# Kernel tuning notes

Hardware: AMD Instinct MI355X
Metric: run time of the kernel (lower is better)

## Reference

```python
import jax, jax.numpy as jnp
import numpy as np

EPS = 1e-5

def _conv3x3(x, w):
    # x: [N,C,H,W], w: [O,I,3,3], stride 1, padding 1
    return jax.lax.conv_general_dilated(
        x, w, window_strides=(1, 1), padding=((1, 1), (1, 1)),
        dimension_numbers=('NCHW', 'OIHW', 'NCHW'))

def _bn(x, gamma, beta, rmean, rvar):
    # inference-mode BatchNorm2d over channel dim
    scale = gamma * jax.lax.rsqrt(rvar + EPS)
    return x * scale[None, :, None, None] + (beta - rmean * scale)[None, :, None, None]

def setup_inputs() -> dict:
    key = jax.random.key(0)
    ks = jax.random.split(key, 8)
    N, C, H, W = 32, 256, 56, 56
    x = jax.random.normal(ks[0], (N, C, H, W), dtype=jnp.float32)
    w1 = jax.random.normal(ks[1], (C, C, 3, 3), dtype=jnp.float32) * 0.05
    w2 = jax.random.normal(ks[2], (C, C, 3, 3), dtype=jnp.float32) * 0.05
    g1 = jax.random.normal(ks[3], (C,), dtype=jnp.float32) * 0.1 + 1.0
    b1 = jax.random.normal(ks[4], (C,), dtype=jnp.float32) * 0.1
    g2 = jax.random.normal(ks[5], (C,), dtype=jnp.float32) * 0.1 + 1.0
    b2 = jax.random.normal(ks[6], (C,), dtype=jnp.float32) * 0.1
    rm1 = jax.random.normal(jax.random.fold_in(key, 10), (C,), dtype=jnp.float32) * 0.1
    rv1 = jax.random.uniform(jax.random.fold_in(key, 11), (C,), dtype=jnp.float32) + 0.5
    rm2 = jax.random.normal(jax.random.fold_in(key, 12), (C,), dtype=jnp.float32) * 0.1
    rv2 = jax.random.uniform(jax.random.fold_in(key, 13), (C,), dtype=jnp.float32) + 0.5
    return {'x': x, 'w1': w1, 'g1': g1, 'b1': b1, 'rm1': rm1, 'rv1': rv1,
            'w2': w2, 'g2': g2, 'b2': b2, 'rm2': rm2, 'rv2': rv2}

def reference(x, w1, g1, b1, rm1, rv1, w2, g2, b2, rm2, rv2):
    identity = x
    out = jax.nn.relu(_bn(_conv3x3(x, w1), g1, b1, rm1, rv1))
    out = _bn(_conv3x3(out, w2), g2, b2, rm2, rv2)
    return jax.nn.relu(out + identity)
```

## Files before the change

### kernel.cpp

```cpp
#include <hip/hip_runtime.h>
#include <hip/hip_bf16.h>

#define NN 32
#define CC 256
#define HH 56
#define WW 56
#define HP 58
#define PIX (HH * WW)
#define MTOT (NN * PIX)
#define BN_EPS 1e-5f

using f32x4  = __attribute__((ext_vector_type(4))) float;
using short8 = __attribute__((ext_vector_type(8))) short;

__device__ __forceinline__ void gload16(const void* g, void* l) {
    __builtin_amdgcn_global_load_lds(
        (const __attribute__((address_space(1))) void*)g,
        (__attribute__((address_space(3))) void*)l, 16, 0, 0);
}


__global__ __launch_bounds__(256) void transform_x(const float* __restrict__ x,
                                                   __hip_bfloat16* __restrict__ xt) {
    __shared__ float t[64][65];
    const int tx = threadIdx.x & 63, ty = threadIdx.x >> 6;
    const int c0 = blockIdx.x * 64, h = blockIdx.y, n = blockIdx.z;
    #pragma unroll
    for (int i = 0; i < 16; ++i) {
        const int c = ty + i * 4;
        float v = 0.f;
        if (tx < WW) v = x[(((size_t)n * CC + c0 + c) * HH + h) * WW + tx];
        t[c][tx] = v;
    }
    __syncthreads();
    #pragma unroll
    for (int i = 0; i < 16; ++i) {
        const int w = ty + i * 4;
        if (w < WW)
            xt[((n * HP + h + 1) * HP + (w + 1)) * CC + c0 + tx] = __float2bfloat16(t[tx][w]);
    }
}

__global__ void transform_w(const float* __restrict__ w, __hip_bfloat16* __restrict__ wt) {
    const int co = blockIdx.x, tap = blockIdx.y, ci = threadIdx.x;
    wt[(tap * CC + co) * CC + ci] = __float2bfloat16(w[(co * CC + ci) * 9 + tap]);
}

__global__ void zero_borders(__hip_bfloat16* __restrict__ buf) {
    const int i = blockIdx.x, n = blockIdx.y;
    int h, w;
    if (i < 58)       { h = 0;              w = i; }
    else if (i < 116) { h = 57;             w = i - 58; }
    else if (i < 172) { h = 1 + (i - 116);  w = 0; }
    else              { h = 1 + (i - 172);  w = 57; }
    buf[((n * HP + h) * HP + w) * CC + threadIdx.x] = __float2bfloat16(0.f);
}

template<bool SECOND>
__global__ __launch_bounds__(256, 4) void conv_mfma(
    const __hip_bfloat16* __restrict__ act,
    const __hip_bfloat16* __restrict__ wt,
    const float* __restrict__ g, const float* __restrict__ bb,
    const float* __restrict__ rm, const float* __restrict__ rv,
    const float* __restrict__ identity,
    void* __restrict__ out)
{
    __shared__ short As[128 * 64];
    __shared__ short Bs[128 * 64];

    const int tid  = threadIdx.x;
    const int lane = tid & 63;
    const int wid  = tid >> 6;
    const int wm = wid >> 1, wn = wid & 1;

    const int bid     = blockIdx.x;
    const int logical = (bid & 7) * 196 + (bid >> 3);
    const int nb = logical & 1;
    const int mb = logical >> 1;

    const int scol = (lane & 7) ^ (lane >> 3);

    int abase[4], bbase[4];
    #pragma unroll
    for (int j = 0; j < 4; ++j) {
        const int r = wid * 32 + j * 8 + (lane >> 3);
        const int p = mb * 128 + r;
        const int n   = p / PIX;
        const int rem = p - n * PIX;
        const int h = rem / WW, w = rem - h * WW;
        abase[j] = (((n * HP + h) * HP + w) * CC + scol * 8) * 2;
        const int co = nb * 128 + r;
        bbase[j] = (co * CC + scol * 8) * 2;
    }

    f32x4 acc[4][4];
    #pragma unroll
    for (int i = 0; i < 4; ++i)
        #pragma unroll
        for (int j = 0; j < 4; ++j)
            acc[i][j] = (f32x4){0.f, 0.f, 0.f, 0.f};

    const char* actB = (const char*)act;
    const char* wtB  = (const char*)wt;
    char* AsL = (char*)As;
    char* BsL = (char*)Bs;

    const int rlane = lane & 15;
    const int xorb  = (rlane & 7) << 4;
    const int colb  = (lane >> 4) << 4;

    for (int cic = 0; cic < 4; ++cic) {
        #pragma unroll
        for (int tap = 0; tap < 9; ++tap) {
            const int dh = tap / 3, dw = tap - dh * 3;
            const int aoff = (dh * HP + dw) * (CC * 2) + cic * 128;
            const int boff = tap * (CC * CC * 2) + cic * 128;
            #pragma unroll
            for (int j = 0; j < 4; ++j) {
                gload16(actB + abase[j] + aoff, AsL + wid * 4096 + j * 1024);
                gload16(wtB  + bbase[j] + boff, BsL + wid * 4096 + j * 1024);
            }
            __syncthreads();
            __builtin_amdgcn_s_setprio(1);
            #pragma unroll
            for (int ks = 0; ks < 2; ++ks) {
                const int coladdr = (ks * 64 + colb) ^ xorb;
                short8 a[4], bq[4];
                #pragma unroll
                for (int mf = 0; mf < 4; ++mf)
                    a[mf] = *(const short8*)(AsL + (wm * 64 + mf * 16 + rlane) * 128 + coladdr);
                #pragma unroll
                for (int nf = 0; nf < 4; ++nf)
                    bq[nf] = *(const short8*)(BsL + (wn * 64 + nf * 16 + rlane) * 128 + coladdr);
                #pragma unroll
                for (int mf = 0; mf < 4; ++mf)
                    #pragma unroll
                    for (int nf = 0; nf < 4; ++nf)
                        acc[mf][nf] = __builtin_amdgcn_mfma_f32_16x16x32_bf16(
                            a[mf], bq[nf], acc[mf][nf], 0, 0, 0);
            }
            __builtin_amdgcn_s_setprio(0);
            __syncthreads();
        }
    }

    const int lm = lane >> 4, ln = lane & 15;
    #pragma unroll
    for (int nf = 0; nf < 4; ++nf) {
        const int co = nb * 128 + wn * 64 + nf * 16 + ln;
        const float scale = g[co] * rsqrtf(rv[co] + BN_EPS);
        const float bias  = bb[co] - rm[co] * scale;
        #pragma unroll
        for (int mf = 0; mf < 4; ++mf) {
            const int p0  = mb * 128 + wm * 64 + mf * 16 + lm * 4;
            const int n   = p0 / PIX;
            const int pr  = p0 - n * PIX;
            f32x4 v = acc[mf][nf];
            if (SECOND) {
                const size_t off = (size_t)(n * CC + co) * PIX + pr;
                const float4 id = *(const float4*)(identity + off);
                float4 o;
                o.x = fmaxf(fmaf(v[0], scale, bias) + id.x, 0.f);
                o.y = fmaxf(fmaf(v[1], scale, bias) + id.y, 0.f);
                o.z = fmaxf(fmaf(v[2], scale, bias) + id.z, 0.f);
                o.w = fmaxf(fmaf(v[3], scale, bias) + id.w, 0.f);
                *(float4*)((float*)out + off) = o;
            } else {
                const int h = pr / WW, w = pr - h * WW;
                __hip_bfloat16* yp = (__hip_bfloat16*)out
                    + ((n * HP + h + 1) * HP + (w + 1)) * CC + co;
                #pragma unroll
                for (int r = 0; r < 4; ++r)
                    yp[r * CC] = __float2bfloat16(fmaxf(fmaf(v[r], scale, bias), 0.f));
            }
        }
    }
}

__device__ __forceinline__ float rb_(float v) { return __bfloat162float(__float2bfloat16(v)); }

template<bool SECOND>
__global__ __launch_bounds__(256) void conv_bn_naive(
    const void* __restrict__ in_v, const float* __restrict__ wmat,
    const float* __restrict__ g, const float* __restrict__ b,
    const float* __restrict__ rm, const float* __restrict__ rv,
    const float* __restrict__ identity, void* __restrict__ out_v)
{
    constexpr int CI_CHUNK = 8;
    __shared__ float xs[CI_CHUNK][3][58];
    __shared__ float ws_s[4][CI_CHUNK][9];
    const int tid = threadIdx.x;
    const int co_l = tid >> 6;
    const int wl_raw = tid & 63;
    const int wl = wl_raw < (WW - 1) ? wl_raw : (WW - 1);
    const int co = blockIdx.x * 4 + co_l;
    const int h = blockIdx.y, n = blockIdx.z;
    const float* in_f = (const float*)in_v;
    const __hip_bfloat16* in_b = (const __hip_bfloat16*)in_v;
    float acc = 0.f;
    for (int ci0 = 0; ci0 < CC; ci0 += CI_CHUNK) {
        __syncthreads();
        for (int i = tid; i < CI_CHUNK * 3 * 58; i += 256) {
            int ci = i / 174, rem = i - ci * 174, r = rem / 58, col = rem - r * 58;
            int h_in = h + r - 1, x_col = col - 1;
            float v = 0.f;
            if ((unsigned)h_in < HH && (unsigned)x_col < WW) {
                int idx = ((n * CC + ci0 + ci) * HH + h_in) * WW + x_col;
                v = SECOND ? __bfloat162float(in_b[idx]) : rb_(in_f[idx]);
            }
            xs[ci][r][col] = v;
        }
        for (int i = tid; i < 4 * CI_CHUNK * 9; i += 256) {
            int c_l = i / (CI_CHUNK * 9), rem = i - c_l * (CI_CHUNK * 9);
            int ci = rem / 9, k = rem - ci * 9;
            ws_s[c_l][ci][k] = rb_(wmat[(blockIdx.x * 4 + c_l) * CC * 9 + (ci0 + ci) * 9 + k]);
        }
        __syncthreads();
        #pragma unroll
        for (int ci = 0; ci < CI_CHUNK; ++ci) {
            float wr[9];
            #pragma unroll
            for (int k = 0; k < 9; ++k) wr[k] = ws_s[co_l][ci][k];
            #pragma unroll
            for (int dh = 0; dh < 3; ++dh)
                #pragma unroll
                for (int dw = 0; dw < 3; ++dw)
                    acc += xs[ci][dh][wl + dw] * wr[dh * 3 + dw];
        }
    }
    if (wl_raw < WW) {
        float scale = g[co] * rsqrtf(rv[co] + BN_EPS);
        float bias = b[co] - rm[co] * scale;
        float v = acc * scale + bias;
        int oidx = ((n * CC + co) * HH + h) * WW + wl_raw;
        if (SECOND) {
            v += identity[oidx];
            ((float*)out_v)[oidx] = fmaxf(v, 0.f);
        } else {
            ((__hip_bfloat16*)out_v)[oidx] = __float2bfloat16(fmaxf(v, 0.f));
        }
    }
}

extern "C" void kernel_launch(void* const* d_in, const int* in_sizes, int n_in,
                              void* d_out, int out_size, void* d_ws, size_t ws_size,
                              hipStream_t stream) {
    const float* x   = (const float*)d_in[0];
    const float* w1  = (const float*)d_in[1];
    const float* g1  = (const float*)d_in[2];
    const float* b1  = (const float*)d_in[3];
    const float* rm1 = (const float*)d_in[4];
    const float* rv1 = (const float*)d_in[5];
    const float* w2  = (const float*)d_in[6];
    const float* g2  = (const float*)d_in[7];
    const float* b2  = (const float*)d_in[8];
    const float* rm2 = (const float*)d_in[9];
    const float* rv2 = (const float*)d_in[10];

    const size_t XT_B = (size_t)NN * HP * HP * CC * 2;
    const size_t WT_B = (size_t)9 * CC * CC * 2;
    const size_t NEED = 2 * XT_B + 2 * WT_B;

    if (ws_size < NEED) {
        __hip_bfloat16* tmp = (__hip_bfloat16*)d_ws;
        dim3 grid(CC / 4, HH, NN);
        conv_bn_naive<false><<<grid, 256, 0, stream>>>(x, w1, g1, b1, rm1, rv1, nullptr, tmp);
        conv_bn_naive<true ><<<grid, 256, 0, stream>>>(tmp, w2, g2, b2, rm2, rv2, x, d_out);
        return;
    }

    char* ws = (char*)d_ws;
    __hip_bfloat16* xt  = (__hip_bfloat16*)ws;
    __hip_bfloat16* y1  = (__hip_bfloat16*)(ws + XT_B);
    __hip_bfloat16* wt1 = (__hip_bfloat16*)(ws + 2 * XT_B);
    __hip_bfloat16* wt2 = (__hip_bfloat16*)(ws + 2 * XT_B + WT_B);

    zero_borders<<<dim3(228, NN), 256, 0, stream>>>(xt);
    zero_borders<<<dim3(228, NN), 256, 0, stream>>>(y1);
    transform_x <<<dim3(4, HH, NN), 256, 0, stream>>>(x, xt);
    transform_w <<<dim3(CC, 9), 256, 0, stream>>>(w1, wt1);
    transform_w <<<dim3(CC, 9), 256, 0, stream>>>(w2, wt2);

    conv_mfma<false><<<1568, 256, 0, stream>>>(xt, wt1, g1, b1, rm1, rv1, nullptr, y1);
    conv_mfma<true ><<<1568, 256, 0, stream>>>(y1, wt2, g2, b2, rm2, rv2, x, d_out);
}
```

Before: 314.5 us.

## Use 256x256 tiles with double-buffered LDS pipelining in conv MFMA kernel

The implicit-GEMM conv kernel now uses 512-thread blocks, each computing a 256-pixel by 256-channel tile, which doubles per-wave work and cuts the grid to 392 blocks. Shared memory is double-buffered (128 KB): loads for the next tap and channel chunk are issued in four phases that interleave with MFMA work, with explicit vmcnt waits and barriers replacing the two syncthreads per step. This aims to hide global-to-LDS latency and raise reuse of each loaded tile. The cost is heavy LDS use and larger accumulator register pressure, allowing only one block per CU, and 392 blocks may not fill all CUs evenly.

```diff
diff --git a/kernel.cpp b/kernel.cpp
--- a/kernel.cpp
+++ b/kernel.cpp
@@ -57,7 +57,7 @@
 }
 
 template<bool SECOND>
-__global__ __launch_bounds__(256, 4) void conv_mfma(
+__global__ __launch_bounds__(512, 2) void conv_mfma(
     const __hip_bfloat16* __restrict__ act,
     const __hip_bfloat16* __restrict__ wt,
     const float* __restrict__ g, const float* __restrict__ bb,
@@ -65,94 +65,128 @@
     const float* __restrict__ identity,
     void* __restrict__ out)
 {
-    __shared__ short As[128 * 64];
-    __shared__ short Bs[128 * 64];
+    __shared__ short S[2][2][256][64];
+    char* SB = (char*)S;
 
     const int tid  = threadIdx.x;
     const int lane = tid & 63;
     const int wid  = tid >> 6;
-    const int wm = wid >> 1, wn = wid & 1;
-
-    const int bid     = blockIdx.x;
-    const int logical = (bid & 7) * 196 + (bid >> 3);
-    const int nb = logical & 1;
-    const int mb = logical >> 1;
+    const int wm   = wid >> 2;
+    const int wn   = wid & 3;
+
+    const int bid = blockIdx.x;
+    const int mb  = (bid & 7) * 49 + (bid >> 3);
 
     const int scol = (lane & 7) ^ (lane >> 3);
 
-    int abase[4], bbase[4];
-    #pragma unroll
-    for (int j = 0; j < 4; ++j) {
-        const int r = wid * 32 + j * 8 + (lane >> 3);
-        const int p = mb * 128 + r;
-        const int n   = p / PIX;
-        const int rem = p - n * PIX;
-        const int h = rem / WW, w = rem - h * WW;
-        abase[j] = (((n * HP + h) * HP + w) * CC + scol * 8) * 2;
-        const int co = nb * 128 + r;
-        bbase[j] = (co * CC + scol * 8) * 2;
-    }
-
-    f32x4 acc[4][4];
-    #pragma unroll
-    for (int i = 0; i < 4; ++i)
+    int abase[2][2], bbase[2][2];
+    #pragma unroll
+    for (int h2 = 0; h2 < 2; ++h2)
+        #pragma unroll
+        for (int j = 0; j < 2; ++j) {
+            const int r = h2 * 128 + j * 64 + wid * 8 + (lane >> 3);
+            const int p = mb * 256 + r;
+            const int n   = p / PIX;
+            const int rem = p - n * PIX;
+            const int h = rem / WW, w = rem - h * WW;
+            abase[h2][j] = (((n * HP + h) * HP + w) * CC + scol * 8) * 2;
+            bbase[h2][j] = (r * CC + scol * 8) * 2;
+        }
+
+    f32x4 acc[8][4];
+    #pragma unroll
+    for (int i = 0; i < 8; ++i)
         #pragma unroll
         for (int j = 0; j < 4; ++j)
             acc[i][j] = (f32x4){0.f, 0.f, 0.f, 0.f};
 
     const char* actB = (const char*)act;
     const char* wtB  = (const char*)wt;
-    char* AsL = (char*)As;
-    char* BsL = (char*)Bs;
+
+    auto stageA = [&](int buf, int h2, int t) {
+        const int cic = t / 9, tap = t - cic * 9;
+        const int dh = tap / 3, dw = tap - dh * 3;
+        const int aoff = (dh * HP + dw) * (CC * 2) + cic * 128;
+        char* dst = SB + buf * 65536 + h2 * 16384 + wid * 1024;
+        gload16(actB + abase[h2][0] + aoff, dst);
+        gload16(actB + abase[h2][1] + aoff, dst + 8192);
+    };
+    auto stageB = [&](int buf, int h2, int t) {
+        const int cic = t / 9, tap = t - cic * 9;
+        const int boff = tap * (CC * CC * 2) + cic * 128;
+        char* dst = SB + buf * 65536 + 32768 + h2 * 16384 + wid * 1024;
+        gload16(wtB + bbase[h2][0] + boff, dst);
+        gload16(wtB + bbase[h2][1] + boff, dst + 8192);
+    };
 
     const int rlane = lane & 15;
     const int xorb  = (rlane & 7) << 4;
     const int colb  = (lane >> 4) << 4;
 
-    for (int cic = 0; cic < 4; ++cic) {
-        #pragma unroll
-        for (int tap = 0; tap < 9; ++tap) {
-            const int dh = tap / 3, dw = tap - dh * 3;
-            const int aoff = (dh * HP + dw) * (CC * 2) + cic * 128;
-            const int boff = tap * (CC * CC * 2) + cic * 128;
+    stageA(0, 0, 0); stageA(0, 1, 0); stageB(0, 0, 0); stageB(0, 1, 0);
+
+    short8 bfr[2][4];
+
+    #pragma unroll 1
+    for (int t = 0; t < 36; ++t) {
+        const int cur = t & 1;
+        const bool last = (t == 35);
+        const char* Ab = SB + cur * 65536;
+        const char* Bb = SB + cur * 65536 + 32768;
+        #pragma unroll
+        for (int p = 0; p < 4; ++p) {
+            if (!last) {
+                if      (p == 0) stageA(cur ^ 1, 0, t + 1);
+                else if (p == 1) stageA(cur ^ 1, 1, t + 1);
+                else if (p == 2) stageB(cur ^ 1, 0, t + 1);
+                else             stageB(cur ^ 1, 1, t + 1);
+            }
+            if (p == 0) {
+                if (!last) asm volatile("s_waitcnt vmcnt(2)" ::: "memory");
+                else       asm volatile("s_waitcnt vmcnt(0)" ::: "memory");
+                __builtin_amdgcn_s_barrier();
+                __builtin_amdgcn_sched_barrier(0);
+            }
+            const int coladdr = ((p & 1) * 64 + colb) ^ xorb;
+            short8 afr[4];
             #pragma unroll
-            for (int j = 0; j < 4; ++j) {
-                gload16(actB + abase[j] + aoff, AsL + wid * 4096 + j * 1024);
-                gload16(wtB  + bbase[j] + boff, BsL + wid * 4096 + j * 1024);
-            }
-            __syncthreads();
+            for (int mi = 0; mi < 4; ++mi)
+                afr[mi] = *(const short8*)(Ab
+                    + (wm * 128 + ((p >> 1) * 4 + mi) * 16 + rlane) * 128 + coladdr);
+            if (p < 2) {
+                #pragma unroll
+                for (int nf = 0; nf < 4; ++nf)
+                    bfr[p][nf] = *(const short8*)(Bb
+                        + (wn * 64 + nf * 16 + rlane) * 128 + coladdr);
+            }
+            if (p != 0) {
+                __builtin_amdgcn_sched_barrier(0);
+                __builtin_amdgcn_s_barrier();
+                __builtin_amdgcn_sched_barrier(0);
+            }
             __builtin_amdgcn_s_setprio(1);
             #pragma unroll
-            for (int ks = 0; ks < 2; ++ks) {
-                const int coladdr = (ks * 64 + colb) ^ xorb;
-                short8 a[4], bq[4];
-                #pragma unroll
-                for (int mf = 0; mf < 4; ++mf)
-                    a[mf] = *(const short8*)(AsL + (wm * 64 + mf * 16 + rlane) * 128 + coladdr);
+            for (int mi = 0; mi < 4; ++mi)
                 #pragma unroll
                 for (int nf = 0; nf < 4; ++nf)
-                    bq[nf] = *(const short8*)(BsL + (wn * 64 + nf * 16 + rlane) * 128 + coladdr);
-                #pragma unroll
-                for (int mf = 0; mf < 4; ++mf)
-                    #pragma unroll
-                    for (int nf = 0; nf < 4; ++nf)
-                        acc[mf][nf] = __builtin_amdgcn_mfma_f32_16x16x32_bf16(
-                            a[mf], bq[nf], acc[mf][nf], 0, 0, 0);
-            }
+                    acc[(p >> 1) * 4 + mi][nf] = __builtin_amdgcn_mfma_f32_16x16x32_bf16(
+                        afr[mi], bfr[p & 1][nf], acc[(p >> 1) * 4 + mi][nf], 0, 0, 0);
             __builtin_amdgcn_s_setprio(0);
-            __syncthreads();
+            __builtin_amdgcn_sched_barrier(0);
+            __builtin_amdgcn_s_barrier();
+            __builtin_amdgcn_sched_barrier(0);
         }
     }
 
     const int lm = lane >> 4, ln = lane & 15;
     #pragma unroll
     for (int nf = 0; nf < 4; ++nf) {
-        const int co = nb * 128 + wn * 64 + nf * 16 + ln;
+        const int co = wn * 64 + nf * 16 + ln;
         const float scale = g[co] * rsqrtf(rv[co] + BN_EPS);
         const float bias  = bb[co] - rm[co] * scale;
         #pragma unroll
-        for (int mf = 0; mf < 4; ++mf) {
-            const int p0  = mb * 128 + wm * 64 + mf * 16 + lm * 4;
+        for (int mf = 0; mf < 8; ++mf) {
+            const int p0  = mb * 256 + wm * 128 + mf * 16 + lm * 4;
             const int n   = p0 / PIX;
             const int pr  = p0 - n * PIX;
             f32x4 v = acc[mf][nf];
@@ -281,6 +315,6 @@
     transform_w <<<dim3(CC, 9), 256, 0, stream>>>(w1, wt1);
     transform_w <<<dim3(CC, 9), 256, 0, stream>>>(w2, wt2);
 
-    conv_mfma<false><<<1568, 256, 0, stream>>>(xt, wt1, g1, b1, rm1, rv1, nullptr, y1);
-    conv_mfma<true ><<<1568, 256, 0, stream>>>(y1, wt2, g2, b2, rm2, rv2, x, d_out);
-}
+    conv_mfma<false><<<392, 512, 0, stream>>>(xt, wt1, g1, b1, rm1, rv1, nullptr, y1);
+    conv_mfma<true ><<<392, 512, 0, stream>>>(y1, wt2, g2, b2, rm2, rv2, x, d_out);
+}
```

Result: slower. 353.1 us (+12.3%).

## Double-buffer LDS tiles with half-depth K chunks to overlap loads and MFMA

Applied to the files above, without the earlier changes.

Splits each K step from 64 to 32 input channels and uses two LDS buffers of the same total size, so the global-to-LDS load for the next (channel chunk, tap) step is issued before computing on the current buffer. This drops one barrier per step and hides global load latency behind MFMA work, with a new swizzled LDS layout to match. In exchange it doubles the number of iterations, and with them the barrier count and loop overhead, and each step has less compute to cover the load.

```diff
diff --git a/kernel.cpp b/kernel.cpp
--- a/kernel.cpp
+++ b/kernel.cpp
@@ -65,8 +65,7 @@
     const float* __restrict__ identity,
     void* __restrict__ out)
 {
-    __shared__ short As[128 * 64];
-    __shared__ short Bs[128 * 64];
+    __shared__ char LDSm[32768];
 
     const int tid  = threadIdx.x;
     const int lane = tid & 63;
@@ -78,19 +77,20 @@
     const int nb = logical & 1;
     const int mb = logical >> 1;
 
-    const int scol = (lane & 7) ^ (lane >> 3);
-
-    int abase[4], bbase[4];
-    #pragma unroll
-    for (int j = 0; j < 4; ++j) {
-        const int r = wid * 32 + j * 8 + (lane >> 3);
-        const int p = mb * 128 + r;
+    const int u_s = (lane & 7) ^ (lane >> 3);
+    const int q_s = u_s & 3;
+
+    int abase[2], bbase[2];
+    #pragma unroll
+    for (int j = 0; j < 2; ++j) {
+        const int prow = wid * 32 + j * 16 + 2 * (lane >> 3) + (u_s >> 2);
+        const int p = mb * 128 + prow;
         const int n   = p / PIX;
         const int rem = p - n * PIX;
         const int h = rem / WW, w = rem - h * WW;
-        abase[j] = (((n * HP + h) * HP + w) * CC + scol * 8) * 2;
-        const int co = nb * 128 + r;
-        bbase[j] = (co * CC + scol * 8) * 2;
+        abase[j] = (((n * HP + h) * HP + w) * CC) * 2 + q_s * 16;
+        const int co = nb * 128 + prow;
+        bbase[j] = co * (CC * 2) + q_s * 16;
     }
 
     f32x4 acc[4][4];
@@ -102,44 +102,55 @@
 
     const char* actB = (const char*)act;
     const char* wtB  = (const char*)wt;
-    char* AsL = (char*)As;
-    char* BsL = (char*)Bs;
-
-    const int rlane = lane & 15;
-    const int xorb  = (rlane & 7) << 4;
-    const int colb  = (lane >> 4) << 4;
-
-    for (int cic = 0; cic < 4; ++cic) {
-        #pragma unroll
-        for (int tap = 0; tap < 9; ++tap) {
-            const int dh = tap / 3, dw = tap - dh * 3;
-            const int aoff = (dh * HP + dw) * (CC * 2) + cic * 128;
-            const int boff = tap * (CC * CC * 2) + cic * 128;
+
+    auto stage = [&](int bufSel, int cic, int tap) {
+        const int dh = tap / 3, dw = tap - dh * 3;
+        const int aoff = (dh * HP + dw) * (CC * 2) + cic * 64;
+        const int boff = tap * (CC * CC * 2) + cic * 64;
+        char* da = LDSm + bufSel * 8192 + wid * 2048;
+        char* db = LDSm + 16384 + bufSel * 8192 + wid * 2048;
+        #pragma unroll
+        for (int j = 0; j < 2; ++j) {
+            gload16(actB + abase[j] + aoff, da + j * 1024);
+            gload16(wtB  + bbase[j] + boff, db + j * 1024);
+        }
+    };
+
+    const int qr = lane >> 4, rr = lane & 15;
+    const int rb_l = ((rr >> 1) << 7) + (((((rr & 1) << 2) + qr) ^ (rr >> 1)) << 4);
+
+    auto compute = [&](int bufSel) {
+        const char* Ab = LDSm + bufSel * 8192;
+        const char* Bb = LDSm + 16384 + bufSel * 8192;
+        short8 a[4], bq[4];
+        #pragma unroll
+        for (int mf = 0; mf < 4; ++mf)
+            a[mf] = *(const short8*)(Ab + wm * 4096 + mf * 1024 + rb_l);
+        #pragma unroll
+        for (int nf = 0; nf < 4; ++nf)
+            bq[nf] = *(const short8*)(Bb + wn * 4096 + nf * 1024 + rb_l);
+        __builtin_amdgcn_s_setprio(1);
+        #pragma unroll
+        for (int mf = 0; mf < 4; ++mf)
             #pragma unroll
-            for (int j = 0; j < 4; ++j) {
-                gload16(actB + abase[j] + aoff, AsL + wid * 4096 + j * 1024);
-                gload16(wtB  + bbase[j] + boff, BsL + wid * 4096 + j * 1024);
+            for (int nf = 0; nf < 4; ++nf)
+                acc[mf][nf] = __builtin_amdgcn_mfma_f32_16x16x32_bf16(
+                    a[mf], bq[nf], acc[mf][nf], 0, 0, 0);
+        __builtin_amdgcn_s_setprio(0);
+    };
+
+    stage(0, 0, 0);
+    __syncthreads();
+    int tg = 0;
+    for (int cic = 0; cic < 8; ++cic) {
+        #pragma unroll
+        for (int tap = 0; tap < 9; ++tap, ++tg) {
+            const int buf = tg & 1;
+            if (tg < 71) {
+                const int tn = tg + 1;
+                stage(buf ^ 1, tn / 9, tn - (tn / 9) * 9);
             }
-            __syncthreads();
-            __builtin_amdgcn_s_setprio(1);
-            #pragma unroll
-            for (int ks = 0; ks < 2; ++ks) {
-                const int coladdr = (ks * 64 + colb) ^ xorb;
-                short8 a[4], bq[4];
-                #pragma unroll
-                for (int mf = 0; mf < 4; ++mf)
-                    a[mf] = *(const short8*)(AsL + (wm * 64 + mf * 16 + rlane) * 128 + coladdr);
-                #pragma unroll
-                for (int nf = 0; nf < 4; ++nf)
-                    bq[nf] = *(const short8*)(BsL + (wn * 64 + nf * 16 + rlane) * 128 + coladdr);
-                #pragma unroll
-                for (int mf = 0; mf < 4; ++mf)
-                    #pragma unroll
-                    for (int nf = 0; nf < 4; ++nf)
-                        acc[mf][nf] = __builtin_amdgcn_mfma_f32_16x16x32_bf16(
-                            a[mf], bq[nf], acc[mf][nf], 0, 0, 0);
-            }
-            __builtin_amdgcn_s_setprio(0);
+            compute(buf);
             __syncthreads();
         }
     }
```

Result: slower. 393.7 us (+25.2%).

## Stage conv1 epilogue through LDS for coalesced stores; fold border zeroing into transform

Applied to the files above, without the earlier changes.

The first conv's epilogue now writes its bf16 results into a swizzled LDS tile, then each thread stores 128-byte contiguous channel runs per pixel. This replaces the scattered 2-byte stores that strided by CC. The transform_x kernel now covers the padded height and width and writes the zero borders itself, which removes one zero_borders launch. The cost is an extra __syncthreads plus LDS round-trip in the epilogue, and the A/B LDS buffers are merged into one array so they can be reused for it.

```diff
diff --git a/kernel.cpp b/kernel.cpp
--- a/kernel.cpp
+++ b/kernel.cpp
@@ -25,19 +25,25 @@
     __shared__ float t[64][65];
     const int tx = threadIdx.x & 63, ty = threadIdx.x >> 6;
     const int c0 = blockIdx.x * 64, h = blockIdx.y, n = blockIdx.z;
-    #pragma unroll
-    for (int i = 0; i < 16; ++i) {
-        const int c = ty + i * 4;
-        float v = 0.f;
-        if (tx < WW) v = x[(((size_t)n * CC + c0 + c) * HH + h) * WW + tx];
-        t[c][tx] = v;
+    const bool hIn = (h >= 1) && (h <= HH);
+    if (hIn) {
+        #pragma unroll
+        for (int i = 0; i < 16; ++i) {
+            const int c = ty + i * 4;
+            float v = 0.f;
+            if (tx < WW) v = x[(((size_t)n * CC + c0 + c) * HH + (h - 1)) * WW + tx];
+            t[c][tx] = v;
+        }
     }
     __syncthreads();
     #pragma unroll
     for (int i = 0; i < 16; ++i) {
-        const int w = ty + i * 4;
-        if (w < WW)
-            xt[((n * HP + h + 1) * HP + (w + 1)) * CC + c0 + tx] = __float2bfloat16(t[tx][w]);
+        const int w0 = ty + i * 4;
+        if (w0 < HP) {
+            float v = 0.f;
+            if (hIn && w0 >= 1 && w0 <= WW) v = t[tx][w0 - 1];
+            xt[((n * HP + h) * HP + w0) * CC + c0 + tx] = __float2bfloat16(v);
+        }
     }
 }
 
@@ -65,8 +71,7 @@
     const float* __restrict__ identity,
     void* __restrict__ out)
 {
-    __shared__ short As[128 * 64];
-    __shared__ short Bs[128 * 64];
+    __shared__ short LDSall[2 * 128 * 64];
 
     const int tid  = threadIdx.x;
     const int lane = tid & 63;
@@ -102,8 +107,8 @@
 
     const char* actB = (const char*)act;
     const char* wtB  = (const char*)wt;
-    char* AsL = (char*)As;
-    char* BsL = (char*)Bs;
+    char* AsL = (char*)LDSall;
+    char* BsL = AsL + 16384;
 
     const int rlane = lane & 15;
     const int xorb  = (rlane & 7) << 4;
@@ -145,18 +150,18 @@
     }
 
     const int lm = lane >> 4, ln = lane & 15;
-    #pragma unroll
-    for (int nf = 0; nf < 4; ++nf) {
-        const int co = nb * 128 + wn * 64 + nf * 16 + ln;
-        const float scale = g[co] * rsqrtf(rv[co] + BN_EPS);
-        const float bias  = bb[co] - rm[co] * scale;
-        #pragma unroll
-        for (int mf = 0; mf < 4; ++mf) {
-            const int p0  = mb * 128 + wm * 64 + mf * 16 + lm * 4;
-            const int n   = p0 / PIX;
-            const int pr  = p0 - n * PIX;
-            f32x4 v = acc[mf][nf];
-            if (SECOND) {
+    if (SECOND) {
+        #pragma unroll
+        for (int nf = 0; nf < 4; ++nf) {
+            const int co = nb * 128 + wn * 64 + nf * 16 + ln;
+            const float scale = g[co] * rsqrtf(rv[co] + BN_EPS);
+            const float bias  = bb[co] - rm[co] * scale;
+            #pragma unroll
+            for (int mf = 0; mf < 4; ++mf) {
+                const int p0  = mb * 128 + wm * 64 + mf * 16 + lm * 4;
+                const int n   = p0 / PIX;
+                const int pr  = p0 - n * PIX;
+                f32x4 v = acc[mf][nf];
                 const size_t off = (size_t)(n * CC + co) * PIX + pr;
                 const float4 id = *(const float4*)(identity + off);
                 float4 o;
@@ -165,14 +170,42 @@
                 o.z = fmaxf(fmaf(v[2], scale, bias) + id.z, 0.f);
                 o.w = fmaxf(fmaf(v[3], scale, bias) + id.w, 0.f);
                 *(float4*)((float*)out + off) = o;
-            } else {
-                const int h = pr / WW, w = pr - h * WW;
-                __hip_bfloat16* yp = (__hip_bfloat16*)out
-                    + ((n * HP + h + 1) * HP + (w + 1)) * CC + co;
-                #pragma unroll
-                for (int r = 0; r < 4; ++r)
-                    yp[r * CC] = __float2bfloat16(fmaxf(fmaf(v[r], scale, bias), 0.f));
-            }
+            }
+        }
+    } else {
+        char* T = (char*)LDSall;
+        #pragma unroll
+        for (int nf = 0; nf < 4; ++nf) {
+            const int co_l = wn * 64 + nf * 16 + ln;
+            const int co_g = nb * 128 + co_l;
+            const float scale = g[co_g] * rsqrtf(rv[co_g] + BN_EPS);
+            const float bias  = bb[co_g] - rm[co_g] * scale;
+            #pragma unroll
+            for (int mf = 0; mf < 4; ++mf) {
+                const int pbase = wm * 64 + mf * 16 + lm * 4;
+                f32x4 v = acc[mf][nf];
+                #pragma unroll
+                for (int r = 0; r < 4; ++r) {
+                    const int p = pbase + r;
+                    const int off = p * 256 + ((co_l * 2) ^ ((p & 7) << 4));
+                    *(__hip_bfloat16*)(T + off) =
+                        __float2bfloat16(fmaxf(fmaf(v[r], scale, bias), 0.f));
+                }
+            }
+        }
+        __syncthreads();
+        const int p  = tid >> 1;
+        const int hf = tid & 1;
+        const int P  = mb * 128 + p;
+        const int n  = P / PIX;
+        const int pr = P - n * PIX;
+        const int h = pr / WW, w = pr - h * WW;
+        __hip_bfloat16* dst = (__hip_bfloat16*)out
+            + ((n * HP + h + 1) * HP + (w + 1)) * CC + nb * 128 + hf * 64;
+        #pragma unroll
+        for (int j = 0; j < 8; ++j) {
+            const int src = p * 256 + ((hf * 128 + j * 16) ^ ((p & 7) << 4));
+            *(float4*)((char*)dst + j * 16) = *(const float4*)(T + src);
         }
     }
 }
@@ -275,9 +308,8 @@
     __hip_bfloat16* wt1 = (__hip_bfloat16*)(ws + 2 * XT_B);
     __hip_bfloat16* wt2 = (__hip_bfloat16*)(ws + 2 * XT_B + WT_B);
 
-    zero_borders<<<dim3(228, NN), 256, 0, stream>>>(xt);
     zero_borders<<<dim3(228, NN), 256, 0, stream>>>(y1);
-    transform_x <<<dim3(4, HH, NN), 256, 0, stream>>>(x, xt);
+    transform_x <<<dim3(4, HP, NN), 256, 0, stream>>>(x, xt);
     transform_w <<<dim3(CC, 9), 256, 0, stream>>>(w1, wt1);
     transform_w <<<dim3(CC, 9), 256, 0, stream>>>(w2, wt2);
 
```

After: 323.3 us. +2.8%, slower.
